# Kernel tuning notes

Measured on AMD Instinct MI355X. Metric: run time of the kernel, lower is better.

## Reference

```python
import jax, jax.numpy as jnp
import numpy as np


def setup_inputs() -> dict:
    key = jax.random.key(0)
    k0, k1, k2, k3, k4 = jax.random.split(key, 5)
    B, S, H, I, E = 4, 2048, 1024, 3584, 8
    scale = 0.02
    return {
        "hidden_states": jax.random.normal(k0, (B, S, H), jnp.float32),
        "gate_w": jax.random.normal(k1, (E, H), jnp.float32) * scale,
        "Wg": jax.random.normal(k2, (E, I, H), jnp.float32) * scale,
        "Wu": jax.random.normal(k3, (E, I, H), jnp.float32) * scale,
        "Wd": jax.random.normal(k4, (E, H, I), jnp.float32) * scale,
        "top_k": 2,
    }


def reference(hidden_states, gate_w, Wg, Wu, Wd, top_k):
    B, S, H = hidden_states.shape
    E = gate_w.shape[0]
    x = hidden_states.reshape(-1, H)  # [N, H]

    # Router: softmax in float32 (matches torch dtype=torch.float), then top-k + renorm.
    router_logits = x @ gate_w.T  # [N, E]
    routing_probs = jax.nn.softmax(router_logits.astype(jnp.float32), axis=-1)
    top_w, sel = jax.lax.top_k(routing_probs, top_k)  # [N, K]
    top_w = top_w / jnp.sum(top_w, axis=-1, keepdims=True)
    top_w = top_w.astype(x.dtype)

    # Combined per-token weight for each expert: sum of top-k weights routed to it.
    # comb[n, e] = sum_k top_w[n, k] * (sel[n, k] == e)
    comb = jnp.einsum("nk,nke->ne", top_w, jax.nn.one_hot(sel, E, dtype=x.dtype))

    out = jnp.zeros_like(x)
    for e in range(E):  # fixed small loop over experts (structurally distinct weights)
        h = jax.nn.silu(x @ Wg[e].T) * (x @ Wu[e].T)  # [N, I] SwiGLU
        out = out + (h @ Wd[e].T) * comb[:, e:e + 1]
    return out.reshape(B, S, H), router_logits
```

## Files before the change

kernel.cpp:

```cpp
#include <hip/hip_runtime.h>
#include <hip/hip_bf16.h>

#define N_TOK 8192
#define H_DIM 1024
#define I_DIM 3584
#define N_EXP 8
#define N_PAIR (N_TOK * 2)

#define BM 256
#define BN 128
#define BK 32
#define MAX_TILES 72

#define NPAN1 (I_DIM / BN)
#define NPAN2 (H_DIM / BN)
#define NWG1  (MAX_TILES * NPAN1)
#define NWG2  (MAX_TILES * NPAN2)

typedef short bf16x8 __attribute__((ext_vector_type(8)));
typedef float f32x4 __attribute__((ext_vector_type(4)));

#define CFENCE() asm volatile("" ::: "memory")

#define WS_CNT      0
#define WS_FILL     64
#define WS_OFF      128
#define WS_NTILES   192
#define WS_TILETAB  256
#define WS_SEL      2048
#define WS_WGT      (WS_SEL    + 2 * N_TOK * 4)
#define WS_PTOK     (WS_WGT    + 2 * N_TOK * 4)
#define WS_PW       (WS_PTOK   + N_PAIR * 4)
#define WS_XBF      (WS_PW     + N_PAIR * 4)
#define WS_HBUF     (WS_XBF    + (size_t)N_TOK * H_DIM * 2)
#define WBF_ELEMS   ((size_t)N_EXP * I_DIM * H_DIM)
#define WS_WGBF     (WS_HBUF + (size_t)N_PAIR * I_DIM * 2)
#define WS_WUBF     (WS_WGBF + WBF_ELEMS * 2)
#define WS_END      (WS_WUBF + WBF_ELEMS * 2)

__device__ __forceinline__ unsigned short f2bf(float f) {
  unsigned int u = __float_as_uint(f);
  unsigned int r = (u + 0x7fffu + ((u >> 16) & 1u)) >> 16;
  return (unsigned short)r;
}

__device__ __forceinline__ uint4 pack8(float4 a, float4 b) {
  uint4 r;
  r.x = (unsigned)f2bf(a.x) | ((unsigned)f2bf(a.y) << 16);
  r.y = (unsigned)f2bf(a.z) | ((unsigned)f2bf(a.w) << 16);
  r.z = (unsigned)f2bf(b.x) | ((unsigned)f2bf(b.y) << 16);
  r.w = (unsigned)f2bf(b.z) | ((unsigned)f2bf(b.w) << 16);
  return r;
}

__device__ __forceinline__ void gll16(const ushort* g, ushort* l) {
  __builtin_amdgcn_global_load_lds(
      (const __attribute__((address_space(1))) unsigned int*)g,
      (__attribute__((address_space(3))) unsigned int*)l, 16, 0, 0);
}

__global__ __launch_bounds__(64) void k_router(
    const float* __restrict__ x, const float* __restrict__ gw,
    float* __restrict__ logits, int* __restrict__ sel,
    float* __restrict__ wgt, int* __restrict__ cnt,
    ushort* __restrict__ xbf)
{
  const int n = blockIdx.x;
  const int lane = threadIdx.x;
  const float4* xr = (const float4*)(x + (size_t)n * H_DIM + lane * 16);
  float4 x0 = xr[0], x1 = xr[1], x2 = xr[2], x3 = xr[3];

  uint4* xo = (uint4*)(xbf + (size_t)n * H_DIM + lane * 16);
  xo[0] = pack8(x0, x1);
  xo[1] = pack8(x2, x3);

  float l[N_EXP];
#pragma unroll
  for (int e = 0; e < N_EXP; ++e) {
    const float4* wr = (const float4*)(gw + e * H_DIM + lane * 16);
    float4 w0 = wr[0], w1 = wr[1], w2 = wr[2], w3 = wr[3];
    float p = x0.x * w0.x + x0.y * w0.y + x0.z * w0.z + x0.w * w0.w
            + x1.x * w1.x + x1.y * w1.y + x1.z * w1.z + x1.w * w1.w
            + x2.x * w2.x + x2.y * w2.y + x2.z * w2.z + x2.w * w2.w
            + x3.x * w3.x + x3.y * w3.y + x3.z * w3.z + x3.w * w3.w;
#pragma unroll
    for (int o = 32; o >= 1; o >>= 1) p += __shfl_xor(p, o, 64);
    l[e] = p;
  }
  float m = l[0];
#pragma unroll
  for (int e = 1; e < N_EXP; ++e) m = fmaxf(m, l[e]);
  float pr[N_EXP]; float den = 0.f;
#pragma unroll
  for (int e = 0; e < N_EXP; ++e) { pr[e] = expf(l[e] - m); den += pr[e]; }
#pragma unroll
  for (int e = 0; e < N_EXP; ++e) pr[e] /= den;
  int i0 = 0; float p0 = pr[0];
#pragma unroll
  for (int e = 1; e < N_EXP; ++e) { if (pr[e] > p0) { p0 = pr[e]; i0 = e; } }
  int i1 = -1; float p1 = -1.f;
#pragma unroll
  for (int e = 0; e < N_EXP; ++e) { if (e != i0 && pr[e] > p1) { p1 = pr[e]; i1 = e; } }
  float rs = 1.f / (p0 + p1);
  if (lane == 0) {
    float* lo = logits + (size_t)n * N_EXP;
#pragma unroll
    for (int e = 0; e < N_EXP; ++e) lo[e] = l[e];
    sel[2 * n] = i0; sel[2 * n + 1] = i1;
    wgt[2 * n] = p0 * rs; wgt[2 * n + 1] = p1 * rs;
    atomicAdd(&cnt[i0], 1);
    atomicAdd(&cnt[i1], 1);
  }
}

__global__ void k_prefix(const int* __restrict__ cnt, int* __restrict__ off,
                         int* __restrict__ ntiles, int* __restrict__ tab)
{
  if (threadIdx.x != 0 || blockIdx.x != 0) return;
  int acc = 0, nt = 0;
  for (int e = 0; e < N_EXP; ++e) {
    off[e] = acc;
    int c = cnt[e];
    for (int r = 0; r < c; r += BM) {
      tab[nt * 3 + 0] = e;
      tab[nt * 3 + 1] = acc + r;
      tab[nt * 3 + 2] = (c - r < BM) ? (c - r) : BM;
      nt++;
    }
    acc += c;
  }
  off[N_EXP] = acc;
  *ntiles = nt;
}

__global__ __launch_bounds__(256) void k_scatter(
    const int* __restrict__ sel, const float* __restrict__ wgt,
    const int* __restrict__ off, int* __restrict__ fill,
    int* __restrict__ ptok, float* __restrict__ pw)
{
  int n = blockIdx.x * 256 + threadIdx.x;
  if (n >= N_TOK) return;
#pragma unroll
  for (int k = 0; k < 2; ++k) {
    int e = sel[2 * n + k];
    int pos = atomicAdd(&fill[e], 1);
    int row = off[e] + pos;
    ptok[row] = n;
    pw[row] = wgt[2 * n + k];
  }
}

__global__ __launch_bounds__(256) void k_cvtw(const float* __restrict__ src,
                                              ushort* __restrict__ dst)
{
  size_t i = (size_t)blockIdx.x * 256 + threadIdx.x;
  const float4* s = (const float4*)(src + i * 8);
  float4 a = s[0], b = s[1];
  ((uint4*)dst)[i] = pack8(a, b);
}


__global__ __launch_bounds__(512) void k_mlp1b(
    const ushort* __restrict__ Wg, const ushort* __restrict__ Wu,
    const ushort* __restrict__ xbf, const int* __restrict__ ptok,
    const int* __restrict__ ntiles, const int* __restrict__ tab,
    ushort* __restrict__ hbuf)
{
  __shared__ ushort sA[2][BM * BK];
  __shared__ ushort sG[2][BN * BK];
  __shared__ ushort sU[2][BN * BK];
  __shared__ int stok[BM];

  const int orig = blockIdx.x;
  const int lin = (orig & 7) * (NWG1 >> 3) + (orig >> 3);
  const int tile = lin / NPAN1;
  const int i0 = (lin % NPAN1) * BN;

  if (tile >= *ntiles) return;
  const int e = tab[tile * 3 + 0];
  const int row0 = tab[tile * 3 + 1];
  const int nrows = tab[tile * 3 + 2];
  const int t = threadIdx.x;

  if (t < BM) {
    int tt = t < nrows ? t : (nrows - 1);
    stok[t] = ptok[row0 + tt];
  }
  __syncthreads();

  const int ak = (t & 3) * 8;
  const int ar = t >> 2;
  const ushort* ga0 = xbf + (size_t)stok[ar] * H_DIM + ak;
  const ushort* ga1 = xbf + (size_t)stok[128 + ar] * H_DIM + ak;

  const ushort* gg0 = Wg + (size_t)e * I_DIM * H_DIM + (size_t)(i0 + ar) * H_DIM + ak;
  const ushort* gu0 = Wu + (size_t)e * I_DIM * H_DIM + (size_t)(i0 + ar) * H_DIM + ak;

  const int lane = t & 63, wid = t >> 6;
  const int wm = wid >> 1, wn = wid & 1;
  const int fr = lane & 15, fq = lane >> 4;

  f32x4 ag[4][4], au[4][4];
#pragma unroll
  for (int m = 0; m < 4; ++m)
#pragma unroll
    for (int n = 0; n < 4; ++n) { ag[m][n] = (f32x4){0,0,0,0}; au[m][n] = (f32x4){0,0,0,0}; }

#define STAGE1(b, kt) do {                      \
    gll16(ga0 + (kt), &sA[b][t * 8]);           \
    gll16(ga1 + (kt), &sA[b][(512 + t) * 8]);   \
    gll16(gg0 + (kt), &sG[b][t * 8]);           \
    gll16(gu0 + (kt), &sU[b][t * 8]);           \
  } while (0)

#define COMPUTE1(b) do {                                                     \
    bf16x8 a[4], bg[4], bu[4];                                               \
    _Pragma("unroll")                                                        \
    for (int m = 0; m < 4; ++m)                                              \
      a[m] = *(const bf16x8*)(&sA[b][(wm * 64 + m * 16 + fr) * BK + fq * 8]);\
    _Pragma("unroll")                                                        \
    for (int n = 0; n < 4; ++n) {                                            \
      bg[n] = *(const bf16x8*)(&sG[b][(wn * 64 + n * 16 + fr) * BK + fq * 8]);\
      bu[n] = *(const bf16x8*)(&sU[b][(wn * 64 + n * 16 + fr) * BK + fq * 8]);\
    }                                                                        \
    _Pragma("unroll")                                                        \
    for (int m = 0; m < 4; ++m)                                              \
      _Pragma("unroll")                                                      \
      for (int n = 0; n < 4; ++n) {                                          \
        ag[m][n] = __builtin_amdgcn_mfma_f32_16x16x32_bf16(a[m], bg[n], ag[m][n], 0, 0, 0); \
        au[m][n] = __builtin_amdgcn_mfma_f32_16x16x32_bf16(a[m], bu[n], au[m][n], 0, 0, 0); \
      }                                                                      \
  } while (0)

  const int NK = H_DIM / BK;
  STAGE1(0, 0);
  CFENCE();
  STAGE1(1, BK);
#pragma unroll 2
  for (int ki = 0; ki < NK - 2; ++ki) {
    const int cur = ki & 1;
    asm volatile("s_waitcnt vmcnt(4)" ::: "memory");
    __builtin_amdgcn_s_barrier();
    CFENCE();
    __builtin_amdgcn_sched_barrier(0);
    COMPUTE1(cur);
    asm volatile("s_waitcnt lgkmcnt(0)" ::: "memory");
    __builtin_amdgcn_sched_barrier(0);
    __builtin_amdgcn_s_barrier();
    CFENCE();
    STAGE1(cur, (ki + 2) * BK);
  }
  asm volatile("s_waitcnt vmcnt(4)" ::: "memory");
  __builtin_amdgcn_s_barrier();
  CFENCE();
  __builtin_amdgcn_sched_barrier(0);
  COMPUTE1(0);
  CFENCE();
  asm volatile("s_waitcnt vmcnt(0) lgkmcnt(0)" ::: "memory");
  __builtin_amdgcn_s_barrier();
  CFENCE();
  __builtin_amdgcn_sched_barrier(0);
  COMPUTE1(1);
#undef STAGE1
#undef COMPUTE1

#pragma unroll
  for (int m = 0; m < 4; ++m) {
    const int rb = wm * 64 + m * 16 + fq * 4;
#pragma unroll
    for (int n = 0; n < 4; ++n) {
      const int col = i0 + wn * 64 + n * 16 + fr;
#pragma unroll
      for (int r = 0; r < 4; ++r) {
        const int row = rb + r;
        if (row < nrows) {
          float g = ag[m][n][r], u = au[m][n][r];
          float hv = (g / (1.f + __expf(-g))) * u;
          hbuf[(size_t)(row0 + row) * I_DIM + col] = f2bf(hv);
        }
      }
    }
  }
}

__global__ __launch_bounds__(512) void k_mlp2b(
    const ushort* __restrict__ Wd, const ushort* __restrict__ hbuf,
    const int* __restrict__ ptok, const float* __restrict__ pw,
    const int* __restrict__ ntiles, const int* __restrict__ tab,
    float* __restrict__ out)
{
  __shared__ ushort sA[2][BM * BK];
  __shared__ ushort sB[2][BN * BK];
  __shared__ int stok[BM];
  __shared__ float sw[BM];

  const int orig = blockIdx.x;
  const int lin = (orig & 7) * (NWG2 >> 3) + (orig >> 3);
  const int tile = lin / NPAN2;
  const int j0 = (lin % NPAN2) * BN;

  if (tile >= *ntiles) return;
  const int e = tab[tile * 3 + 0];
  const int row0 = tab[tile * 3 + 1];
  const int nrows = tab[tile * 3 + 2];
  const int t = threadIdx.x;

  if (t < BM) {
    int tt = t < nrows ? t : (nrows - 1);
    stok[t] = ptok[row0 + tt];
    sw[t] = pw[row0 + tt];
  }
  __syncthreads();

  const int ak = (t & 3) * 8;
  const int ar = t >> 2;
  int arow0 = row0 + ar;        if (arow0 > N_PAIR - 1) arow0 = N_PAIR - 1;
  int arow1 = row0 + 128 + ar;  if (arow1 > N_PAIR - 1) arow1 = N_PAIR - 1;
  const ushort* ga0 = hbuf + (size_t)arow0 * I_DIM + ak;
  const ushort* ga1 = hbuf + (size_t)arow1 * I_DIM + ak;

  const ushort* gb0 = Wd + (size_t)e * H_DIM * I_DIM + (size_t)(j0 + ar) * I_DIM + ak;

  const int lane = t & 63, wid = t >> 6;
  const int wm = wid >> 1, wn = wid & 1;
  const int fr = lane & 15, fq = lane >> 4;

  f32x4 ac[4][4];
#pragma unroll
  for (int m = 0; m < 4; ++m)
#pragma unroll
    for (int n = 0; n < 4; ++n) ac[m][n] = (f32x4){0,0,0,0};

#define STAGE2(b, kt) do {                      \
    gll16(ga0 + (kt), &sA[b][t * 8]);           \
    gll16(ga1 + (kt), &sA[b][(512 + t) * 8]);   \
    gll16(gb0 + (kt), &sB[b][t * 8]);           \
  } while (0)

#define COMPUTE2(b) do {                                                     \
    bf16x8 a[4], bb[4];                                                      \
    _Pragma("unroll")                                                        \
    for (int m = 0; m < 4; ++m)                                              \
      a[m] = *(const bf16x8*)(&sA[b][(wm * 64 + m * 16 + fr) * BK + fq * 8]);\
    _Pragma("unroll")                                                        \
    for (int n = 0; n < 4; ++n)                                              \
      bb[n] = *(const bf16x8*)(&sB[b][(wn * 64 + n * 16 + fr) * BK + fq * 8]);\
    _Pragma("unroll")                                                        \
    for (int m = 0; m < 4; ++m)                                              \
      _Pragma("unroll")                                                      \
      for (int n = 0; n < 4; ++n)                                            \
        ac[m][n] = __builtin_amdgcn_mfma_f32_16x16x32_bf16(a[m], bb[n], ac[m][n], 0, 0, 0); \
  } while (0)

  const int NK = I_DIM / BK;
  STAGE2(0, 0);
  CFENCE();
  STAGE2(1, BK);
#pragma unroll 2
  for (int ki = 0; ki < NK - 2; ++ki) {
    const int cur = ki & 1;
    asm volatile("s_waitcnt vmcnt(3)" ::: "memory");
    __builtin_amdgcn_s_barrier();
    CFENCE();
    __builtin_amdgcn_sched_barrier(0);
    COMPUTE2(cur);
    asm volatile("s_waitcnt lgkmcnt(0)" ::: "memory");
    __builtin_amdgcn_sched_barrier(0);
    __builtin_amdgcn_s_barrier();
    CFENCE();
    STAGE2(cur, (ki + 2) * BK);
  }
  asm volatile("s_waitcnt vmcnt(3)" ::: "memory");
  __builtin_amdgcn_s_barrier();
  CFENCE();
  __builtin_amdgcn_sched_barrier(0);
  COMPUTE2(0);
  CFENCE();
  asm volatile("s_waitcnt vmcnt(0) lgkmcnt(0)" ::: "memory");
  __builtin_amdgcn_s_barrier();
  CFENCE();
  __builtin_amdgcn_sched_barrier(0);
  COMPUTE2(1);
#undef STAGE2
#undef COMPUTE2

#pragma unroll
  for (int m = 0; m < 4; ++m) {
    const int rb = wm * 64 + m * 16 + fq * 4;
#pragma unroll
    for (int n = 0; n < 4; ++n) {
      const int col = j0 + wn * 64 + n * 16 + fr;
#pragma unroll
      for (int r = 0; r < 4; ++r) {
        const int row = rb + r;
        if (row < nrows) {
          float v = ac[m][n][r] * sw[row];
          atomicAdd(&out[(size_t)stok[row] * H_DIM + col], v);
        }
      }
    }
  }
}


#define FBM 128

__global__ __launch_bounds__(256) void k_mlp1(
    const float* __restrict__ Wg, const float* __restrict__ Wu,
    const ushort* __restrict__ xbf, const int* __restrict__ ptok,
    const int* __restrict__ ntiles, const int* __restrict__ tab,
    ushort* __restrict__ hbuf)
{
  __shared__ ushort sA[FBM * BK];
  __shared__ ushort sG[BN * BK];
  __shared__ ushort sU[BN * BK];
  __shared__ int stok[FBM];

  const int tile = blockIdx.x;
  if (tile >= *ntiles) return;
  const int e = tab[tile * 3 + 0];
  const int row0 = tab[tile * 3 + 1] + (blockIdx.z ? FBM : 0);
  int nrows = tab[tile * 3 + 2] - (blockIdx.z ? FBM : 0);
  if (nrows <= 0) return;
  if (nrows > FBM) nrows = FBM;
  const int i0 = blockIdx.y * BN;
  const int t = threadIdx.x;

  if (t < FBM) {
    int tt = t < nrows ? t : (nrows - 1);
    stok[t] = ptok[row0 + tt];
  }
  __syncthreads();

  const int ak = (t & 3) * 8;
  const ushort* ga0 = xbf + (size_t)stok[t >> 2] * H_DIM + ak;
  const ushort* ga1 = xbf + (size_t)stok[64 + (t >> 2)] * H_DIM + ak;
  ushort* la0 = sA + (size_t)t * 8;
  ushort* la1 = sA + (size_t)(256 + t) * 8;

  const int wr = t >> 1, wcb = (t & 1) * 16;
  const float* gwg = Wg + (size_t)e * I_DIM * H_DIM + (size_t)(i0 + wr) * H_DIM + wcb;
  const float* gwu = Wu + (size_t)e * I_DIM * H_DIM + (size_t)(i0 + wr) * H_DIM + wcb;
  ushort* lwg = sG + wr * BK + wcb;
  ushort* lwu = sU + wr * BK + wcb;

  const int lane = t & 63, wid = t >> 6;
  const int wm = wid >> 1, wn = wid & 1;
  const int fr = lane & 15, fq = lane >> 4;

  f32x4 ag[4][4], au[4][4];
#pragma unroll
  for (int m = 0; m < 4; ++m)
#pragma unroll
    for (int n = 0; n < 4; ++n) { ag[m][n] = (f32x4){0,0,0,0}; au[m][n] = (f32x4){0,0,0,0}; }

  for (int kt = 0; kt < H_DIM; kt += BK) {
    gll16(ga0 + kt, la0);
    gll16(ga1 + kt, la1);

    const float4* pg = (const float4*)(gwg + kt);
    const float4* pu = (const float4*)(gwu + kt);
    float4 g0 = pg[0], g1 = pg[1], g2 = pg[2], g3 = pg[3];
    float4 u0 = pu[0], u1 = pu[1], u2 = pu[2], u3 = pu[3];
    ((uint4*)lwg)[0] = pack8(g0, g1);
    ((uint4*)lwg)[1] = pack8(g2, g3);
    ((uint4*)lwu)[0] = pack8(u0, u1);
    ((uint4*)lwu)[1] = pack8(u2, u3);
    __syncthreads();

    bf16x8 a[4], bg[4], bu[4];
#pragma unroll
    for (int m = 0; m < 4; ++m)
      a[m] = *(const bf16x8*)(sA + (wm * 64 + m * 16 + fr) * BK + fq * 8);
#pragma unroll
    for (int n = 0; n < 4; ++n) {
      bg[n] = *(const bf16x8*)(sG + (wn * 64 + n * 16 + fr) * BK + fq * 8);
      bu[n] = *(const bf16x8*)(sU + (wn * 64 + n * 16 + fr) * BK + fq * 8);
    }
#pragma unroll
    for (int m = 0; m < 4; ++m)
#pragma unroll
      for (int n = 0; n < 4; ++n) {
        ag[m][n] = __builtin_amdgcn_mfma_f32_16x16x32_bf16(a[m], bg[n], ag[m][n], 0, 0, 0);
        au[m][n] = __builtin_amdgcn_mfma_f32_16x16x32_bf16(a[m], bu[n], au[m][n], 0, 0, 0);
      }
    __syncthreads();
  }

#pragma unroll
  for (int m = 0; m < 4; ++m) {
    const int rb = wm * 64 + m * 16 + fq * 4;
#pragma unroll
    for (int n = 0; n < 4; ++n) {
      const int col = i0 + wn * 64 + n * 16 + fr;
#pragma unroll
      for (int r = 0; r < 4; ++r) {
        const int row = rb + r;
        if (row < nrows) {
          float g = ag[m][n][r], u = au[m][n][r];
          float hv = (g / (1.f + __expf(-g))) * u;
          hbuf[(size_t)(row0 + row) * I_DIM + col] = f2bf(hv);
        }
      }
    }
  }
}

__global__ __launch_bounds__(256) void k_mlp2(
    const float* __restrict__ Wd, const ushort* __restrict__ hbuf,
    const int* __restrict__ ptok, const float* __restrict__ pw,
    const int* __restrict__ ntiles, const int* __restrict__ tab,
    float* __restrict__ out)
{
  __shared__ ushort sA[FBM * BK];
  __shared__ ushort sB[BN * BK];
  __shared__ int stok[FBM];
  __shared__ float sw[FBM];

  const int tile = blockIdx.x;
  if (tile >= *ntiles) return;
  const int e = tab[tile * 3 + 0];
  const int row0 = tab[tile * 3 + 1] + (blockIdx.z ? FBM : 0);
  int nrows = tab[tile * 3 + 2] - (blockIdx.z ? FBM : 0);
  if (nrows <= 0) return;
  if (nrows > FBM) nrows = FBM;
  const int j0 = blockIdx.y * BN;
  const int t = threadIdx.x;

  if (t < FBM) {
    int tt = t < nrows ? t : (nrows - 1);
    stok[t] = ptok[row0 + tt];
    sw[t] = pw[row0 + tt];
  }
  __syncthreads();

  const int ak = (t & 3) * 8;
  int arow0 = row0 + (t >> 2);       if (arow0 > N_PAIR - 1) arow0 = N_PAIR - 1;
  int arow1 = row0 + 64 + (t >> 2);  if (arow1 > N_PAIR - 1) arow1 = N_PAIR - 1;
  const ushort* ga0 = hbuf + (size_t)arow0 * I_DIM + ak;
  const ushort* ga1 = hbuf + (size_t)arow1 * I_DIM + ak;
  ushort* la0 = sA + (size_t)t * 8;
  ushort* la1 = sA + (size_t)(256 + t) * 8;

  const int wr = t >> 1, wcb = (t & 1) * 16;
  const float* gb = Wd + (size_t)e * H_DIM * I_DIM + (size_t)(j0 + wr) * I_DIM + wcb;
  ushort* lb = sB + wr * BK + wcb;

  const int lane = t & 63, wid = t >> 6;
  const int wm = wid >> 1, wn = wid & 1;
  const int fr = lane & 15, fq = lane >> 4;

  f32x4 ac[4][4];
#pragma unroll
  for (int m = 0; m < 4; ++m)
#pragma unroll
    for (int n = 0; n < 4; ++n) ac[m][n] = (f32x4){0,0,0,0};

  for (int kt = 0; kt < I_DIM; kt += BK) {
    gll16(ga0 + kt, la0);
    gll16(ga1 + kt, la1);

    const float4* pb = (const float4*)(gb + kt);
    float4 b0 = pb[0], b1 = pb[1], b2 = pb[2], b3 = pb[3];
    ((uint4*)lb)[0] = pack8(b0, b1);
    ((uint4*)lb)[1] = pack8(b2, b3);
    __syncthreads();

    bf16x8 a[4], bb[4];
#pragma unroll
    for (int m = 0; m < 4; ++m)
      a[m] = *(const bf16x8*)(sA + (wm * 64 + m * 16 + fr) * BK + fq * 8);
#pragma unroll
    for (int n = 0; n < 4; ++n)
      bb[n] = *(const bf16x8*)(sB + (wn * 64 + n * 16 + fr) * BK + fq * 8);
#pragma unroll
    for (int m = 0; m < 4; ++m)
#pragma unroll
      for (int n = 0; n < 4; ++n)
        ac[m][n] = __builtin_amdgcn_mfma_f32_16x16x32_bf16(a[m], bb[n], ac[m][n], 0, 0, 0);
    __syncthreads();
  }

#pragma unroll
  for (int m = 0; m < 4; ++m) {
    const int rb = wm * 64 + m * 16 + fq * 4;
#pragma unroll
    for (int n = 0; n < 4; ++n) {
      const int col = j0 + wn * 64 + n * 16 + fr;
#pragma unroll
      for (int r = 0; r < 4; ++r) {
        const int row = rb + r;
        if (row < nrows) {
          float v = ac[m][n][r] * sw[row];
          atomicAdd(&out[(size_t)stok[row] * H_DIM + col], v);
        }
      }
    }
  }
}

extern "C" void kernel_launch(void* const* d_in, const int* in_sizes, int n_in,
                              void* d_out, int out_size, void* d_ws, size_t ws_size,
                              hipStream_t stream)
{
  const float* x  = (const float*)d_in[0];
  const float* gw = (const float*)d_in[1];
  const float* Wg = (const float*)d_in[2];
  const float* Wu = (const float*)d_in[3];
  const float* Wd = (const float*)d_in[4];

  float* out    = (float*)d_out;
  float* logits = out + (size_t)N_TOK * H_DIM;

  char* ws = (char*)d_ws;
  int*    cnt    = (int*)(ws + WS_CNT);
  int*    fill   = (int*)(ws + WS_FILL);
  int*    off    = (int*)(ws + WS_OFF);
  int*    ntiles = (int*)(ws + WS_NTILES);
  int*    tab    = (int*)(ws + WS_TILETAB);
  int*    sel    = (int*)(ws + WS_SEL);
  float*  wgt    = (float*)(ws + WS_WGT);
  int*    ptok   = (int*)(ws + WS_PTOK);
  float*  pw     = (float*)(ws + WS_PW);
  ushort* xbf    = (ushort*)(ws + WS_XBF);
  ushort* hbuf   = (ushort*)(ws + WS_HBUF);
  ushort* wgbf   = (ushort*)(ws + WS_WGBF);
  ushort* wubf   = (ushort*)(ws + WS_WUBF);
  ushort* wdbf   = wgbf;

  const bool fast = (ws_size >= WS_END);

  hipMemsetAsync(d_out, 0, (size_t)N_TOK * H_DIM * sizeof(float), stream);
  hipMemsetAsync(ws, 0, 128, stream);

  k_router<<<N_TOK, 64, 0, stream>>>(x, gw, logits, sel, wgt, cnt, xbf);
  k_prefix<<<1, 64, 0, stream>>>(cnt, off, ntiles, tab);
  k_scatter<<<N_TOK / 256, 256, 0, stream>>>(sel, wgt, off, fill, ptok, pw);

  const int cvtblocks = (int)(WBF_ELEMS / 8 / 256);

  if (fast) {
    k_cvtw<<<cvtblocks, 256, 0, stream>>>(Wg, wgbf);
    k_cvtw<<<cvtblocks, 256, 0, stream>>>(Wu, wubf);
    k_mlp1b<<<NWG1, 512, 0, stream>>>(wgbf, wubf, xbf, ptok, ntiles, tab, hbuf);
    k_cvtw<<<cvtblocks, 256, 0, stream>>>(Wd, wdbf);
    k_mlp2b<<<NWG2, 512, 0, stream>>>(wdbf, hbuf, ptok, pw, ntiles, tab, out);
  } else {
    dim3 gA(MAX_TILES, I_DIM / BN, 2);
    dim3 gB(MAX_TILES, H_DIM / BN, 2);
    k_mlp1<<<gA, 256, 0, stream>>>(Wg, Wu, xbf, ptok, ntiles, tab, hbuf);
    k_mlp2<<<gB, 256, 0, stream>>>(Wd, hbuf, ptok, pw, ntiles, tab, out);
  }
}
```

Measured before the change: 980.1 us.

## Widen expert GEMM tiles to 256x256 with 1024-thread blocks and split-K down-proj

Doubles the N-dimension tile of both expert GEMMs to 256, so each 1024-thread workgroup (16 waves in a 4x4 grid, still 64x64 per wave) covers a 256x256 output tile and reuses each loaded A row across twice as many columns. The down-projection kernel also splits the I reduction in half across two workgroups to keep enough workgroups in flight for the smaller H dimension. The vmcnt waits are lowered to match the reduced number of global-to-LDS loads per stage. With 1024-thread blocks the per-thread register budget shrinks. The gate/up kernel keeps 128 fp32 accumulator registers per thread, so it risks spilling or low occupancy, and split-K doubles the accumulation traffic into the output.

```diff
diff --git a/kernel.cpp b/kernel.cpp
--- a/kernel.cpp
+++ b/kernel.cpp
@@ -8,14 +8,14 @@
 #define N_PAIR (N_TOK * 2)
 
 #define BM 256
-#define BN 128
+#define BN 256
 #define BK 32
 #define MAX_TILES 72
 
 #define NPAN1 (I_DIM / BN)
 #define NPAN2 (H_DIM / BN)
 #define NWG1  (MAX_TILES * NPAN1)
-#define NWG2  (MAX_TILES * NPAN2)
+#define NWG2  (MAX_TILES * NPAN2 * 2)
 
 typedef short bf16x8 __attribute__((ext_vector_type(8)));
 typedef float f32x4 __attribute__((ext_vector_type(4)));
@@ -160,7 +160,7 @@
 }
 
 
-__global__ __launch_bounds__(512) void k_mlp1b(
+__global__ __launch_bounds__(1024) void k_mlp1b(
     const ushort* __restrict__ Wg, const ushort* __restrict__ Wu,
     const ushort* __restrict__ xbf, const int* __restrict__ ptok,
     const int* __restrict__ ntiles, const int* __restrict__ tab,
@@ -191,13 +191,11 @@
   const int ak = (t & 3) * 8;
   const int ar = t >> 2;
   const ushort* ga0 = xbf + (size_t)stok[ar] * H_DIM + ak;
-  const ushort* ga1 = xbf + (size_t)stok[128 + ar] * H_DIM + ak;
-
   const ushort* gg0 = Wg + (size_t)e * I_DIM * H_DIM + (size_t)(i0 + ar) * H_DIM + ak;
   const ushort* gu0 = Wu + (size_t)e * I_DIM * H_DIM + (size_t)(i0 + ar) * H_DIM + ak;
 
   const int lane = t & 63, wid = t >> 6;
-  const int wm = wid >> 1, wn = wid & 1;
+  const int wm = wid >> 2, wn = wid & 3;
   const int fr = lane & 15, fq = lane >> 4;
 
   f32x4 ag[4][4], au[4][4];
@@ -208,7 +206,6 @@
 
 #define STAGE1(b, kt) do {                      \
     gll16(ga0 + (kt), &sA[b][t * 8]);           \
-    gll16(ga1 + (kt), &sA[b][(512 + t) * 8]);   \
     gll16(gg0 + (kt), &sG[b][t * 8]);           \
     gll16(gu0 + (kt), &sU[b][t * 8]);           \
   } while (0)
@@ -239,7 +236,7 @@
 #pragma unroll 2
   for (int ki = 0; ki < NK - 2; ++ki) {
     const int cur = ki & 1;
-    asm volatile("s_waitcnt vmcnt(4)" ::: "memory");
+    asm volatile("s_waitcnt vmcnt(3)" ::: "memory");
     __builtin_amdgcn_s_barrier();
     CFENCE();
     __builtin_amdgcn_sched_barrier(0);
@@ -250,7 +247,7 @@
     CFENCE();
     STAGE1(cur, (ki + 2) * BK);
   }
-  asm volatile("s_waitcnt vmcnt(4)" ::: "memory");
+  asm volatile("s_waitcnt vmcnt(3)" ::: "memory");
   __builtin_amdgcn_s_barrier();
   CFENCE();
   __builtin_amdgcn_sched_barrier(0);
@@ -283,7 +280,7 @@
   }
 }
 
-__global__ __launch_bounds__(512) void k_mlp2b(
+__global__ __launch_bounds__(1024) void k_mlp2b(
     const ushort* __restrict__ Wd, const ushort* __restrict__ hbuf,
     const int* __restrict__ ptok, const float* __restrict__ pw,
     const int* __restrict__ ntiles, const int* __restrict__ tab,
@@ -296,8 +293,10 @@
 
   const int orig = blockIdx.x;
   const int lin = (orig & 7) * (NWG2 >> 3) + (orig >> 3);
-  const int tile = lin / NPAN2;
-  const int j0 = (lin % NPAN2) * BN;
+  const int tile = lin >> 3;
+  const int rem = lin & 7;
+  const int j0 = (rem >> 1) * BN;
+  const int kz = rem & 1;
 
   if (tile >= *ntiles) return;
   const int e = tab[tile * 3 + 0];
@@ -312,17 +311,17 @@
   }
   __syncthreads();
 
+  const int KHALF = I_DIM / 2;
+  const int kbase = kz * KHALF;
+
   const int ak = (t & 3) * 8;
   const int ar = t >> 2;
   int arow0 = row0 + ar;        if (arow0 > N_PAIR - 1) arow0 = N_PAIR - 1;
-  int arow1 = row0 + 128 + ar;  if (arow1 > N_PAIR - 1) arow1 = N_PAIR - 1;
-  const ushort* ga0 = hbuf + (size_t)arow0 * I_DIM + ak;
-  const ushort* ga1 = hbuf + (size_t)arow1 * I_DIM + ak;
-
-  const ushort* gb0 = Wd + (size_t)e * H_DIM * I_DIM + (size_t)(j0 + ar) * I_DIM + ak;
+  const ushort* ga0 = hbuf + (size_t)arow0 * I_DIM + kbase + ak;
+  const ushort* gb0 = Wd + (size_t)e * H_DIM * I_DIM + (size_t)(j0 + ar) * I_DIM + kbase + ak;
 
   const int lane = t & 63, wid = t >> 6;
-  const int wm = wid >> 1, wn = wid & 1;
+  const int wm = wid >> 2, wn = wid & 3;
   const int fr = lane & 15, fq = lane >> 4;
 
   f32x4 ac[4][4];
@@ -333,7 +332,6 @@
 
 #define STAGE2(b, kt) do {                      \
     gll16(ga0 + (kt), &sA[b][t * 8]);           \
-    gll16(ga1 + (kt), &sA[b][(512 + t) * 8]);   \
     gll16(gb0 + (kt), &sB[b][t * 8]);           \
   } while (0)
 
@@ -352,14 +350,14 @@
         ac[m][n] = __builtin_amdgcn_mfma_f32_16x16x32_bf16(a[m], bb[n], ac[m][n], 0, 0, 0); \
   } while (0)
 
-  const int NK = I_DIM / BK;
+  const int NK = KHALF / BK;
   STAGE2(0, 0);
   CFENCE();
   STAGE2(1, BK);
 #pragma unroll 2
   for (int ki = 0; ki < NK - 2; ++ki) {
     const int cur = ki & 1;
-    asm volatile("s_waitcnt vmcnt(3)" ::: "memory");
+    asm volatile("s_waitcnt vmcnt(2)" ::: "memory");
     __builtin_amdgcn_s_barrier();
     CFENCE();
     __builtin_amdgcn_sched_barrier(0);
@@ -370,7 +368,7 @@
     CFENCE();
     STAGE2(cur, (ki + 2) * BK);
   }
-  asm volatile("s_waitcnt vmcnt(3)" ::: "memory");
+  asm volatile("s_waitcnt vmcnt(2)" ::: "memory");
   __builtin_amdgcn_s_barrier();
   CFENCE();
   __builtin_amdgcn_sched_barrier(0);
@@ -404,6 +402,7 @@
 
 
 #define FBM 128
+#define FBN 128
 
 __global__ __launch_bounds__(256) void k_mlp1(
     const float* __restrict__ Wg, const float* __restrict__ Wu,
@@ -412,8 +411,8 @@
     ushort* __restrict__ hbuf)
 {
   __shared__ ushort sA[FBM * BK];
-  __shared__ ushort sG[BN * BK];
-  __shared__ ushort sU[BN * BK];
+  __shared__ ushort sG[FBN * BK];
+  __shared__ ushort sU[FBN * BK];
   __shared__ int stok[FBM];
 
   const int tile = blockIdx.x;
@@ -423,7 +422,7 @@
   int nrows = tab[tile * 3 + 2] - (blockIdx.z ? FBM : 0);
   if (nrows <= 0) return;
   if (nrows > FBM) nrows = FBM;
-  const int i0 = blockIdx.y * BN;
+  const int i0 = blockIdx.y * FBN;
   const int t = threadIdx.x;
 
   if (t < FBM) {
@@ -513,7 +512,7 @@
     float* __restrict__ out)
 {
   __shared__ ushort sA[FBM * BK];
-  __shared__ ushort sB[BN * BK];
+  __shared__ ushort sB[FBN * BK];
   __shared__ int stok[FBM];
   __shared__ float sw[FBM];
 
@@ -524,7 +523,7 @@
   int nrows = tab[tile * 3 + 2] - (blockIdx.z ? FBM : 0);
   if (nrows <= 0) return;
   if (nrows > FBM) nrows = FBM;
-  const int j0 = blockIdx.y * BN;
+  const int j0 = blockIdx.y * FBN;
   const int t = threadIdx.x;
 
   if (t < FBM) {
@@ -642,12 +641,12 @@
   if (fast) {
     k_cvtw<<<cvtblocks, 256, 0, stream>>>(Wg, wgbf);
     k_cvtw<<<cvtblocks, 256, 0, stream>>>(Wu, wubf);
-    k_mlp1b<<<NWG1, 512, 0, stream>>>(wgbf, wubf, xbf, ptok, ntiles, tab, hbuf);
+    k_mlp1b<<<NWG1, 1024, 0, stream>>>(wgbf, wubf, xbf, ptok, ntiles, tab, hbuf);
     k_cvtw<<<cvtblocks, 256, 0, stream>>>(Wd, wdbf);
-    k_mlp2b<<<NWG2, 512, 0, stream>>>(wdbf, hbuf, ptok, pw, ntiles, tab, out);
+    k_mlp2b<<<NWG2, 1024, 0, stream>>>(wdbf, hbuf, ptok, pw, ntiles, tab, out);
   } else {
-    dim3 gA(MAX_TILES, I_DIM / BN, 2);
-    dim3 gB(MAX_TILES, H_DIM / BN, 2);
+    dim3 gA(MAX_TILES, I_DIM / FBN, 2);
+    dim3 gB(MAX_TILES, H_DIM / FBN, 2);
     k_mlp1<<<gA, 256, 0, stream>>>(Wg, Wu, xbf, ptok, ntiles, tab, hbuf);
     k_mlp2<<<gB, 256, 0, stream>>>(Wd, hbuf, ptok, pw, ntiles, tab, out);
   }
```

New measurement: 3.316 ms. 238% more time.
